# Optimization experiments

Hardware: AMD Instinct MI355X
Metric: run time of the kernel (lower is better)

## Reference

```python
import jax, jax.numpy as jnp
import numpy as np

N, Lq, Lk = 4, 4096, 4096
H, P = 16, 128
D = H * P  # 2048


def setup_inputs() -> dict:
    key = jax.random.key(0)
    ks = jax.random.split(key, 7)
    s = 1.0 / np.sqrt(D).astype(np.float32)
    query = jax.random.normal(ks[0], (N, Lq, D), jnp.float32)
    key_t = jax.random.normal(ks[1], (N, Lk, D), jnp.float32)
    Wq = jax.random.normal(ks[2], (D, D), jnp.float32) * s
    Wk = jax.random.normal(ks[3], (D, D), jnp.float32) * s
    Wv = jax.random.normal(ks[4], (D, D), jnp.float32) * s
    query_padding_mask = jax.random.uniform(ks[5], (N, Lq)) < 0.1
    key_padding_mask = jax.random.uniform(ks[6], (N, Lk)) < 0.1
    return {"query": query, "key": key_t, "Wq": Wq, "Wk": Wk, "Wv": Wv,
            "query_padding_mask": query_padding_mask,
            "key_padding_mask": key_padding_mask}


def reference(query, key, Wq, Wk, Wv, query_padding_mask, key_padding_mask):
    n, lq, _ = query.shape
    lk = key.shape[1]
    # torch.nn.Linear(bias=False): y = x @ W^T; split into heads -> (N,H,L,P)
    q = (query @ Wq.T).reshape(n, lq, H, P).transpose(0, 2, 1, 3)
    k = (key @ Wk.T).reshape(n, lk, H, P).transpose(0, 2, 1, 3)
    v = (key @ Wv.T).reshape(n, lk, H, P).transpose(0, 2, 1, 3)
    # _log_exp_kernel(x) = log(1 + exp(x)) = softplus
    pq = jax.nn.softplus(q)
    pk = jax.nn.softplus(k)
    # zero out padded keys so they contribute nothing to numerator/denominator
    pk = jnp.where(key_padding_mask[:, None, :, None], 0.0, pk)
    # linear attention: O(L*d^2) instead of O(L^2*d)
    kv = jnp.einsum("nhkd,nhke->nhde", pk, v)          # (N,H,P,P)
    num = jnp.einsum("nhqd,nhde->nhqe", pq, kv)        # (N,H,Lq,P)
    den = jnp.einsum("nhqd,nhd->nhq", pq, pk.sum(axis=2))[..., None]
    att = num / den
    out = att.transpose(0, 2, 1, 3).reshape(n, lq, H * P)
    # zero out padded query positions
    out = jnp.where(query_padding_mask[..., None], 0.0, out)
    return out
```

## Files before the change

kernel.cpp:

```cpp
#include <hip/hip_runtime.h>
#include <stdint.h>

typedef __attribute__((ext_vector_type(8))) short    bh8;
typedef __attribute__((ext_vector_type(4))) float    fx4;
typedef __attribute__((ext_vector_type(4))) float    f4v;
typedef unsigned short u16;
typedef __attribute__((ext_vector_type(4))) unsigned short u16x4;

#define DEV static __device__ __forceinline__

DEV u16 f2bf(float f) {
  unsigned u = __float_as_uint(f);
  u += 0x7FFFu + ((u >> 16) & 1u);
  return (u16)(u >> 16);
}
DEV float bf2f(u16 s) { return __uint_as_float(((unsigned)s) << 16); }
DEV float softplus_f(float x) { return fmaxf(x, 0.f) + log1pf(expf(-fabsf(x))); }

DEV void gload_lds16(const u16* g, u16* l) {
  __builtin_amdgcn_global_load_lds(
      (const __attribute__((address_space(1))) unsigned int*)g,
      (__attribute__((address_space(3))) unsigned int*)l, 16, 0, 0);
}
DEV void stage2(const u16* s, u16* d) {
  gload_lds16(s, d);
  gload_lds16(s + 131072, d + 4096);
}

__global__ __launch_bounds__(256) void k_cvt_all(
    const float* __restrict__ q, const float* __restrict__ k,
    const float* __restrict__ wq, const float* __restrict__ wk,
    const float* __restrict__ wv, u16* __restrict__ dst) {
  const int N4 = 19922944;
  int i = blockIdx.x * 256 + threadIdx.x;
  int stride = gridDim.x * 256;
  for (; i < N4; i += stride) {
    const float* src; int off;
    if (i < 8388608)        { src = q;  off = i; }
    else if (i < 16777216)  { src = k;  off = i - 8388608; }
    else if (i < 17825792)  { src = wq; off = i - 16777216; }
    else if (i < 18874368)  { src = wk; off = i - 17825792; }
    else                    { src = wv; off = i - 18874368; }
    f4v v = ((const f4v*)src)[off];
    u16x4 o;
    o.x = f2bf(v.x); o.y = f2bf(v.y); o.z = f2bf(v.z); o.w = f2bf(v.w);
    ((u16x4*)dst)[i] = o;
  }
}


#define MM(a, b, c) __builtin_amdgcn_mfma_f32_16x16x32_bf16(a, b, c, 0, 0, 0)
#define LD(BASE, RR, KS) \
  (*(const bh8*)&lsg[(BASE) + (RR) * 64 + ((((KS) * 32) + ko8) ^ swz)])

#define DECLQ(Q)                                                          \
  fx4 acc##Q##00 = {}, acc##Q##01 = {}, acc##Q##10 = {}, acc##Q##11 = {}, \
      acc##Q##20 = {}, acc##Q##21 = {}, acc##Q##30 = {}, acc##Q##31 = {}

#define DECLFRAGS                                                         \
  bh8 a_00 = {}, a_01 = {}, a_10 = {}, a_11 = {},                         \
      a_20 = {}, a_21 = {}, a_30 = {}, a_31 = {};                         \
  bh8 b0_00 = {}, b0_01 = {}, b0_10 = {}, b0_11 = {};                     \
  bh8 b1_00 = {}, b1_01 = {}, b1_10 = {}, b1_11 = {};

#define LDA4(AB, KS)                                                     \
  a_0##KS = LD(AB, arow0,      KS); a_1##KS = LD(AB, arow0 + 16, KS);    \
  a_2##KS = LD(AB, arow0 + 32, KS); a_3##KS = LD(AB, arow0 + 48, KS);

#define LDB2(BN, BB, KS)                                                 \
  b##BN##_0##KS = LD(BB, brow0,      KS);                                \
  b##BN##_1##KS = LD(BB, brow0 + 16, KS);

#define MFMA8(Q, BN, KS)                                                 \
  acc##Q##00 = MM(a_0##KS, b##BN##_0##KS, acc##Q##00);                   \
  acc##Q##01 = MM(a_0##KS, b##BN##_1##KS, acc##Q##01);                   \
  acc##Q##10 = MM(a_1##KS, b##BN##_0##KS, acc##Q##10);                   \
  acc##Q##11 = MM(a_1##KS, b##BN##_1##KS, acc##Q##11);                   \
  acc##Q##20 = MM(a_2##KS, b##BN##_0##KS, acc##Q##20);                   \
  acc##Q##21 = MM(a_2##KS, b##BN##_1##KS, acc##Q##21);                   \
  acc##Q##30 = MM(a_3##KS, b##BN##_0##KS, acc##Q##30);                   \
  acc##Q##31 = MM(a_3##KS, b##BN##_1##KS, acc##Q##31);

#define KREGION(ABASE, BBASE, DA, DB, SA, SB) {                          \
  stage2(SA,            lsu + (DA));                                     \
  stage2((SA) + 262144, lsu + (DA) + 8192);                              \
  stage2(SB,            lsu + (DB));                                     \
  stage2((SB) + 262144, lsu + (DB) + 8192);                              \
  LDA4(ABASE, 0) LDA4(ABASE, 1)                                          \
  LDB2(0, BBASE, 0) LDB2(0, BBASE, 1)                                    \
  LDB2(1, (BBASE) + 8192, 0) LDB2(1, (BBASE) + 8192, 1)                  \
  __builtin_amdgcn_s_setprio(1);                                         \
  MFMA8(0, 0, 0) MFMA8(0, 0, 1) MFMA8(1, 1, 0) MFMA8(1, 1, 1)            \
  LDA4((ABASE) + 8192, 0) LDA4((ABASE) + 8192, 1)                        \
  MFMA8(2, 0, 0) MFMA8(2, 0, 1) MFMA8(3, 1, 0) MFMA8(3, 1, 1)            \
  __builtin_amdgcn_s_setprio(0);                                         \
  asm volatile("s_waitcnt vmcnt(0)");                                    \
  __builtin_amdgcn_s_barrier();                                          \
}

#define STE(AC, EL, JOFF) {                                                   \
  float v = AC.EL;                                                            \
  if (EPI >= 1) v = softplus_f(v);                                            \
  if (EPI == 2) { if (mask[gi0 + JOFF]) v = 0.f; }                            \
  C[(size_t)(gi0 + JOFF) * 2048 + gj] = f2bf(v);                              \
}
#define ST1(AC, QR, QC, MI, NI) {                                             \
  int gi0 = bm0 + (QR) * 128 + wr * 64 + (MI) * 16 + (lane >> 4) * 4;         \
  int gj  = bn0 + (QC) * 128 + wc * 32 + (NI) * 16 + l15;                     \
  STE(AC, x, 0) STE(AC, y, 1) STE(AC, z, 2) STE(AC, w, 3)                     \
}
#define EPIQ(Q, QR, QC)                                                       \
  ST1(acc##Q##00, QR, QC, 0, 0) ST1(acc##Q##01, QR, QC, 0, 1)                 \
  ST1(acc##Q##10, QR, QC, 1, 0) ST1(acc##Q##11, QR, QC, 1, 1)                 \
  ST1(acc##Q##20, QR, QC, 2, 0) ST1(acc##Q##21, QR, QC, 2, 1)                 \
  ST1(acc##Q##30, QR, QC, 3, 0) ST1(acc##Q##31, QR, QC, 3, 1)

template <int EPI>
__global__ __launch_bounds__(512, 2) void k_gemm256(
    const u16* __restrict__ A, const u16* __restrict__ B, u16* __restrict__ C,
    const int* __restrict__ mask) {
  extern __shared__ u16 lsg[];
  int tid = threadIdx.x, lane = tid & 63, wid = tid >> 6;
  int xcd = blockIdx.x & 7, i = blockIdx.x >> 3;
  int bm0 = (xcd * 8 + (i & 7)) << 8;
  int bn0 = (i >> 3) << 8;
  int wr = wid >> 2, wc = wid & 3;
  int l15 = lane & 15, ko8 = (lane >> 4) * 8;
  int swz = (l15 & 7) << 3;
  int arow0 = wr * 64 + l15, brow0 = wc * 32 + l15;
  int lr = lane >> 3, cg = (lane & 7) ^ lr;
  const u16* srcA = A + (size_t)(bm0 + wid * 8 + lr) * 2048 + cg * 8;
  const u16* srcB = B + (size_t)(bn0 + wid * 8 + lr) * 2048 + cg * 8;
  u16* lsu = lsg + wid * 512;

  DECLQ(0); DECLQ(1); DECLQ(2); DECLQ(3);
  DECLFRAGS

  stage2(srcA,          lsu + 0);
  stage2(srcA + 262144, lsu + 8192);
  stage2(srcB,          lsu + 16384);
  stage2(srcB + 262144, lsu + 24576);
  asm volatile("s_waitcnt vmcnt(0)");
  __builtin_amdgcn_s_barrier();

  for (int it = 0; it < 16; it++) {
    const u16* sA1 = srcA + (2 * it + 1) * 64;
    const u16* sB1 = srcB + (2 * it + 1) * 64;
    int t2 = (2 * it + 2) & 31;
    const u16* sA2 = srcA + t2 * 64;
    const u16* sB2 = srcB + t2 * 64;
    KREGION(0,     16384, 32768, 49152, sA1, sB1)
    KREGION(32768, 49152, 0,     16384, sA2, sB2)
  }

  EPIQ(0, 0, 0)
  EPIQ(1, 0, 1)
  EPIQ(2, 1, 0)
  EPIQ(3, 1, 1)
}

__global__ __launch_bounds__(256, 2) void k_kv2(const u16* __restrict__ pk,
                                                const u16* __restrict__ v,
                                                float* __restrict__ part,
                                                float* __restrict__ spart) {
  int nh = blockIdx.x >> 3, slab = blockIdx.x & 7;
  int n = nh >> 4, h = nh & 15;
  __shared__ u16 lsA[128 * 32];
  __shared__ u16 lsB[128 * 32];
  __shared__ float redS[32][128];
  int tid = threadIdx.x, lane = tid & 63, wid = tid >> 6;
  int wr = wid >> 1, wc = wid & 1;
  int kk = tid >> 3;
  int dg = (tid & 7) * 16;
  size_t rowbase = ((size_t)(n * 4096 + slab * 512) + kk) * 2048 + h * 128 + dg;
  int r = lane & 15, ko = (lane >> 4) * 8;
  fx4 acc[4][4] = {};
  float sA[16];
#pragma unroll
  for (int i = 0; i < 16; i++) sA[i] = 0.f;
  for (int k0 = 0; k0 < 512; k0 += 32) {
    __syncthreads();
    bh8 a0 = *(const bh8*)(pk + rowbase + (size_t)k0 * 2048);
    bh8 a1 = *(const bh8*)(pk + rowbase + (size_t)k0 * 2048 + 8);
    bh8 b0 = *(const bh8*)(v + rowbase + (size_t)k0 * 2048);
    bh8 b1 = *(const bh8*)(v + rowbase + (size_t)k0 * 2048 + 8);
#pragma unroll
    for (int i = 0; i < 8; i++) {
      sA[i] += bf2f((u16)a0[i]);
      sA[8 + i] += bf2f((u16)a1[i]);
    }
#pragma unroll
    for (int i = 0; i < 8; i++) {
      lsA[(dg + i) * 32 + kk] = (u16)a0[i];
      lsA[(dg + 8 + i) * 32 + kk] = (u16)a1[i];
      lsB[(dg + i) * 32 + kk] = (u16)b0[i];
      lsB[(dg + 8 + i) * 32 + kk] = (u16)b1[i];
    }
    __syncthreads();
    bh8 af[4], bfr[4];
#pragma unroll
    for (int mi = 0; mi < 4; mi++)
      af[mi] = *(const bh8*)&lsA[(wr * 64 + mi * 16 + r) * 32 + ko];
#pragma unroll
    for (int ni = 0; ni < 4; ni++)
      bfr[ni] = *(const bh8*)&lsB[(wc * 64 + ni * 16 + r) * 32 + ko];
#pragma unroll
    for (int mi = 0; mi < 4; mi++)
#pragma unroll
      for (int ni = 0; ni < 4; ni++)
        acc[mi][ni] = __builtin_amdgcn_mfma_f32_16x16x32_bf16(af[mi], bfr[ni],
                                                              acc[mi][ni], 0, 0, 0);
  }
#pragma unroll
  for (int mi = 0; mi < 4; mi++)
#pragma unroll
    for (int ni = 0; ni < 4; ni++)
#pragma unroll
      for (int j = 0; j < 4; j++) {
        int d = wr * 64 + mi * 16 + (lane >> 4) * 4 + j;
        int e = wc * 64 + ni * 16 + (lane & 15);
        part[(size_t)blockIdx.x * 16384 + e * 128 + d] = acc[mi][ni][j];
      }
#pragma unroll
  for (int i = 0; i < 16; i++) redS[kk][dg + i] = sA[i];
  __syncthreads();
  if (tid < 128) {
    float s = 0.f;
#pragma unroll
    for (int p = 0; p < 32; p++) s += redS[p][tid];
    spart[blockIdx.x * 128 + tid] = s;
  }
}

__global__ __launch_bounds__(256) void k_red(const float* __restrict__ part,
                                             const float* __restrict__ spart,
                                             u16* __restrict__ kvT,
                                             float* __restrict__ sb) {
  int nh = blockIdx.x, tid = threadIdx.x;
  for (int i = tid; i < 16384; i += 256) {
    float s = 0.f;
#pragma unroll
    for (int sl = 0; sl < 8; sl++) s += part[(size_t)(nh * 8 + sl) * 16384 + i];
    kvT[(size_t)nh * 16384 + i] = f2bf(s);
  }
  if (tid < 128) {
    float s = 0.f;
#pragma unroll
    for (int sl = 0; sl < 8; sl++) s += spart[(nh * 8 + sl) * 128 + tid];
    sb[nh * 128 + tid] = s;
  }
}

__global__ __launch_bounds__(256, 2) void k_att(
    const u16* __restrict__ pq, const u16* __restrict__ kvT,
    const float* __restrict__ s, const int* __restrict__ qmask,
    float* __restrict__ out) {
  int b = blockIdx.x;
  int lt = b & 31, h = (b >> 5) & 15, nb = b >> 9;
  int l0 = lt * 128;
  __shared__ u16 lsQ[128 * 128];
  __shared__ u16 lsKV[128 * 128];
  __shared__ float lsS[128];
  __shared__ float lsDen[128];
  int tid = threadIdx.x, lane = tid & 63, wid = tid >> 6;

  int row = tid >> 1, part = tid & 1;
  const u16* gq = pq + ((size_t)(nb * 4096 + l0 + row)) * 2048 + h * 128 + part * 64;
  const u16* gk = kvT + ((size_t)(nb * 16 + h) * 128 + row) * 128 + part * 64;
  int sw = (row & 7) << 3;
#pragma unroll
  for (int j = 0; j < 8; j++) {
    bh8 vq = *(const bh8*)(gq + j * 8);
    bh8 vk = *(const bh8*)(gk + j * 8);
    int ci = (part * 64 + j * 8) ^ sw;
    *(bh8*)&lsQ[row * 128 + ci] = vq;
    *(bh8*)&lsKV[row * 128 + ci] = vk;
  }
  if (tid < 128) lsS[tid] = s[(nb * 16 + h) * 128 + tid];
  __syncthreads();

  if (tid < 128) {
    int rr = tid, swr = (rr & 7) << 3;
    float dsum = 0.f;
    for (int dd = 0; dd < 128; dd++) {
      int d = (dd + rr) & 127;
      dsum += bf2f(lsQ[rr * 128 + (d ^ swr)]) * lsS[d];
    }
    lsDen[rr] = dsum;
  }
  __syncthreads();

  int wr = wid >> 1, wc = wid & 1;
  int r = lane & 15, ko = (lane >> 4) * 8;
  fx4 acc[4][4] = {};
#pragma unroll
  for (int ks = 0; ks < 4; ks++) {
    bh8 af[4], bfr[4];
#pragma unroll
    for (int mi = 0; mi < 4; mi++) {
      int rw = wr * 64 + mi * 16 + r;
      af[mi] = *(const bh8*)&lsQ[rw * 128 + ((ks * 32 + ko) ^ ((rw & 7) << 3))];
    }
#pragma unroll
    for (int ni = 0; ni < 4; ni++) {
      int rw = wc * 64 + ni * 16 + r;
      bfr[ni] = *(const bh8*)&lsKV[rw * 128 + ((ks * 32 + ko) ^ ((rw & 7) << 3))];
    }
#pragma unroll
    for (int mi = 0; mi < 4; mi++)
#pragma unroll
      for (int ni = 0; ni < 4; ni++)
        acc[mi][ni] = __builtin_amdgcn_mfma_f32_16x16x32_bf16(af[mi], bfr[ni],
                                                              acc[mi][ni], 0, 0, 0);
  }
#pragma unroll
  for (int mi = 0; mi < 4; mi++)
#pragma unroll
    for (int ni = 0; ni < 4; ni++)
#pragma unroll
      for (int j = 0; j < 4; j++) {
        int li = wr * 64 + mi * 16 + (lane >> 4) * 4 + j;
        int e = wc * 64 + ni * 16 + (lane & 15);
        int l = l0 + li;
        float v = qmask[nb * 4096 + l] ? 0.f : acc[mi][ni][j] / lsDen[li];
        out[((size_t)(nb * 4096 + l)) * 2048 + h * 128 + e] = v;
      }
}

extern "C" void kernel_launch(void* const* d_in, const int* in_sizes, int n_in,
                              void* d_out, int out_size, void* d_ws, size_t ws_size,
                              hipStream_t stream) {
  const float* query = (const float*)d_in[0];
  const float* key   = (const float*)d_in[1];
  const float* Wq    = (const float*)d_in[2];
  const float* Wk    = (const float*)d_in[3];
  const float* Wv    = (const float*)d_in[4];
  const int* qmask   = (const int*)d_in[5];
  const int* kmask   = (const int*)d_in[6];
  float* out = (float*)d_out;
  char* ws = (char*)d_ws;

  u16* qb   = (u16*)(ws + 0);
  u16* kb   = (u16*)(ws + 67108864ull);
  u16* Wqb  = (u16*)(ws + 134217728ull);
  u16* Wkb  = (u16*)(ws + 142606336ull);
  u16* Wvb  = (u16*)(ws + 150994944ull);
  u16* pq   = (u16*)(ws + 159383552ull);
  u16* kvT  = (u16*)(ws + 226492416ull);
  float* sb = (float*)(ws + 228589568ull);
  float* kvpart = (float*)(ws + 0);
  float* spart  = (float*)(ws + 33554432ull);
  u16* pk = (u16*)d_out;
  u16* vb = (u16*)d_out + 33554432ull;

  k_cvt_all<<<2048, 256, 0, stream>>>(query, key, Wq, Wk, Wv, qb);

  k_gemm256<1><<<512, 512, 131072, stream>>>(qb, Wqb, pq, nullptr);
  k_gemm256<2><<<512, 512, 131072, stream>>>(kb, Wkb, pk, kmask);
  k_gemm256<0><<<512, 512, 131072, stream>>>(kb, Wvb, vb, nullptr);

  k_kv2<<<512, 256, 0, stream>>>(pk, vb, kvpart, spart);
  k_red<<<64, 256, 0, stream>>>(kvpart, spart, kvT, sb);
  k_att<<<2048, 256, 0, stream>>>(pq, kvT, sb, qmask, out);
}
```

Measured before the change: 732.7 us.

## Add 8-phase ping-pong pipelined GEMM kernel for the query projection

Introduces k_gemm8p, a 256x256-tile bf16 MFMA GEMM that splits each K-step into eight phases. Each phase interleaves LDS fragment reads and the next global-to-LDS stage loads with MFMA bursts, using double-buffered LDS and per-phase barriers. The warp layout gives each wave 128x64 outputs. It replaces the original kernel only for the Q projection, aiming to hide load latency better, at the cost of more barriers and higher register pressure.

```diff
diff --git a/kernel.cpp b/kernel.cpp
--- a/kernel.cpp
+++ b/kernel.cpp
@@ -48,10 +48,139 @@
   }
 }
 
-
 #define MM(a, b, c) __builtin_amdgcn_mfma_f32_16x16x32_bf16(a, b, c, 0, 0, 0)
 #define LD(BASE, RR, KS) \
   (*(const bh8*)&lsg[(BASE) + (RR) * 64 + ((((KS) * 32) + ko8) ^ swz)])
+
+#define STE(AC, EL, JOFF) {                                                   \
+  float v = AC.EL;                                                            \
+  if (EPI >= 1) v = softplus_f(v);                                            \
+  if (EPI == 2) { if (mask[gi0 + JOFF]) v = 0.f; }                            \
+  C[(size_t)(gi0 + JOFF) * 2048 + gj] = f2bf(v);                              \
+}
+
+#define DECLA(G)                                                         \
+  bh8 a##G##_00 = {}, a##G##_01 = {}, a##G##_10 = {}, a##G##_11 = {},    \
+      a##G##_20 = {}, a##G##_21 = {}, a##G##_30 = {}, a##G##_31 = {};
+#define DECLB(J)                                                         \
+  bh8 b##J##_00 = {}, b##J##_01 = {}, b##J##_10 = {}, b##J##_11 = {};
+#define DECLQ8(Q)                                                         \
+  fx4 acc##Q##00 = {}, acc##Q##01 = {}, acc##Q##10 = {}, acc##Q##11 = {}, \
+      acc##Q##20 = {}, acc##Q##21 = {}, acc##Q##30 = {}, acc##Q##31 = {};
+
+#define RDA8(G, BASE, RO)                                                    \
+  a##G##_00 = LD(BASE, arow + (RO),      0);                                 \
+  a##G##_01 = LD(BASE, arow + (RO),      1);                                 \
+  a##G##_10 = LD(BASE, arow + (RO) + 16, 0);                                 \
+  a##G##_11 = LD(BASE, arow + (RO) + 16, 1);                                 \
+  a##G##_20 = LD(BASE, arow + (RO) + 32, 0);                                 \
+  a##G##_21 = LD(BASE, arow + (RO) + 32, 1);                                 \
+  a##G##_30 = LD(BASE, arow + (RO) + 48, 0);                                 \
+  a##G##_31 = LD(BASE, arow + (RO) + 48, 1);
+
+#define RDB4(J, BASE, CO)                                                    \
+  b##J##_00 = LD(BASE, brow + (CO),      0);                                 \
+  b##J##_01 = LD(BASE, brow + (CO),      1);                                 \
+  b##J##_10 = LD(BASE, brow + (CO) + 16, 0);                                 \
+  b##J##_11 = LD(BASE, brow + (CO) + 16, 1);
+
+#define MFQ(G, J, Q)                                                         \
+  acc##Q##00 = MM(a##G##_00, b##J##_00, acc##Q##00);                         \
+  acc##Q##01 = MM(a##G##_00, b##J##_10, acc##Q##01);                         \
+  acc##Q##10 = MM(a##G##_10, b##J##_00, acc##Q##10);                         \
+  acc##Q##11 = MM(a##G##_10, b##J##_10, acc##Q##11);                         \
+  acc##Q##20 = MM(a##G##_20, b##J##_00, acc##Q##20);                         \
+  acc##Q##21 = MM(a##G##_20, b##J##_10, acc##Q##21);                         \
+  acc##Q##30 = MM(a##G##_30, b##J##_00, acc##Q##30);                         \
+  acc##Q##31 = MM(a##G##_30, b##J##_10, acc##Q##31);                         \
+  acc##Q##00 = MM(a##G##_01, b##J##_01, acc##Q##00);                         \
+  acc##Q##01 = MM(a##G##_01, b##J##_11, acc##Q##01);                         \
+  acc##Q##10 = MM(a##G##_11, b##J##_01, acc##Q##10);                         \
+  acc##Q##11 = MM(a##G##_11, b##J##_11, acc##Q##11);                         \
+  acc##Q##20 = MM(a##G##_21, b##J##_01, acc##Q##20);                         \
+  acc##Q##21 = MM(a##G##_21, b##J##_11, acc##Q##21);                         \
+  acc##Q##30 = MM(a##G##_31, b##J##_01, acc##Q##30);                         \
+  acc##Q##31 = MM(a##G##_31, b##J##_11, acc##Q##31);
+
+#define PH8(MFMAS, PRE, ...) {                  \
+  PRE                                           \
+  __VA_ARGS__                                   \
+  __builtin_amdgcn_s_barrier();                 \
+  asm volatile("s_waitcnt lgkmcnt(0)");         \
+  __builtin_amdgcn_s_setprio(1);                \
+  MFMAS                                         \
+  __builtin_amdgcn_s_setprio(0);                \
+}
+#define VM0 asm volatile("s_waitcnt vmcnt(0)");
+
+#define STF(AC, MI, NI, RO, CO) {                                            \
+  int gi0 = bm0 + wr * 128 + (RO) + (MI) * 16 + (lane >> 4) * 4;             \
+  int gj  = bn0 + wc * 64 + (CO) + (NI) * 16 + l15;                          \
+  STE(AC, x, 0) STE(AC, y, 1) STE(AC, z, 2) STE(AC, w, 3)                    \
+}
+#define EPQ8(Q, RO, CO)                                                      \
+  STF(acc##Q##00, 0, 0, RO, CO) STF(acc##Q##01, 0, 1, RO, CO)                \
+  STF(acc##Q##10, 1, 0, RO, CO) STF(acc##Q##11, 1, 1, RO, CO)                \
+  STF(acc##Q##20, 2, 0, RO, CO) STF(acc##Q##21, 2, 1, RO, CO)                \
+  STF(acc##Q##30, 3, 0, RO, CO) STF(acc##Q##31, 3, 1, RO, CO)
+
+template <int EPI>
+__global__ __launch_bounds__(512, 2) void k_gemm8p(
+    const u16* __restrict__ A, const u16* __restrict__ B, u16* __restrict__ C,
+    const int* __restrict__ mask) {
+  extern __shared__ u16 lsg[];
+  int tid = threadIdx.x, lane = tid & 63, wid = tid >> 6;
+  int xcd = blockIdx.x & 7, i = blockIdx.x >> 3;
+  int bm0 = (xcd * 8 + (i & 7)) << 8;
+  int bn0 = (i >> 3) << 8;
+  int wr = wid >> 2, wc = wid & 3;
+  int l15 = lane & 15, ko8 = (lane >> 4) * 8;
+  int swz = (l15 & 7) << 3;
+  int arow = l15;
+  int brow = (wc & 1) * 64 + l15;
+  int abw0 = wr * 8192, abw1 = 32768 + wr * 8192;
+  int bbw0 = 16384 + (wc >> 1) * 8192, bbw1 = 49152 + (wc >> 1) * 8192;
+  int lr = lane >> 3, cg = (lane & 7) ^ lr;
+  const u16* srcA = A + (size_t)(bm0 + wid * 8 + lr) * 2048 + cg * 8;
+  const u16* srcB = B + (size_t)(bn0 + wid * 8 + lr) * 2048 + cg * 8;
+  u16* lsu = lsg + wid * 512;
+
+  DECLQ8(0) DECLQ8(1) DECLQ8(2) DECLQ8(3)
+  DECLA(L) DECLA(H) DECLB(0) DECLB(1)
+
+  stage2(srcA,          lsu + 0);
+  stage2(srcA + 262144, lsu + 8192);
+  stage2(srcB,          lsu + 16384);
+  stage2(srcB + 262144, lsu + 24576);
+  asm volatile("s_waitcnt vmcnt(0)");
+  __builtin_amdgcn_s_barrier();
+
+  for (int it = 0; it < 16; it++) {
+    const u16* sA1 = srcA + (2 * it + 1) * 64;
+    const u16* sB1 = srcB + (2 * it + 1) * 64;
+    int t2 = (2 * it + 2) & 31;
+    const u16* sA2 = srcA + t2 * 64;
+    const u16* sB2 = srcB + t2 * 64;
+    PH8(MFQ(L, 0, 0), ,
+        RDA8(L, abw0, 0) RDB4(0, bbw0, 0)
+        stage2(sA1, lsu + 32768); stage2(sA1 + 262144, lsu + 40960);)
+    PH8(MFQ(L, 1, 1), ,
+        RDB4(1, bbw0, 32)
+        stage2(sB1, lsu + 49152); stage2(sB1 + 262144, lsu + 57344);)
+    PH8(MFQ(H, 0, 2), , RDA8(H, abw0, 64))
+    PH8(MFQ(H, 1, 3), VM0, )
+    PH8(MFQ(L, 0, 0), ,
+        RDA8(L, abw1, 0) RDB4(0, bbw1, 0)
+        stage2(sA2, lsu + 0); stage2(sA2 + 262144, lsu + 8192);)
+    PH8(MFQ(L, 1, 1), ,
+        RDB4(1, bbw1, 32)
+        stage2(sB2, lsu + 16384); stage2(sB2 + 262144, lsu + 24576);)
+    PH8(MFQ(H, 0, 2), , RDA8(H, abw1, 64))
+    PH8(MFQ(H, 1, 3), VM0, )
+  }
+
+  EPQ8(0, 0, 0) EPQ8(1, 0, 32) EPQ8(2, 64, 0) EPQ8(3, 64, 32)
+}
 
 #define DECLQ(Q)                                                          \
   fx4 acc##Q##00 = {}, acc##Q##01 = {}, acc##Q##10 = {}, acc##Q##11 = {}, \
@@ -98,12 +227,6 @@
   __builtin_amdgcn_s_barrier();                                          \
 }
 
-#define STE(AC, EL, JOFF) {                                                   \
-  float v = AC.EL;                                                            \
-  if (EPI >= 1) v = softplus_f(v);                                            \
-  if (EPI == 2) { if (mask[gi0 + JOFF]) v = 0.f; }                            \
-  C[(size_t)(gi0 + JOFF) * 2048 + gj] = f2bf(v);                              \
-}
 #define ST1(AC, QR, QC, MI, NI) {                                             \
   int gi0 = bm0 + (QR) * 128 + wr * 64 + (MI) * 16 + (lane >> 4) * 4;         \
   int gj  = bn0 + (QC) * 128 + wc * 32 + (NI) * 16 + l15;                     \
@@ -355,7 +478,7 @@
 
   k_cvt_all<<<2048, 256, 0, stream>>>(query, key, Wq, Wk, Wv, qb);
 
-  k_gemm256<1><<<512, 512, 131072, stream>>>(qb, Wqb, pq, nullptr);
+  k_gemm8p<1><<<512, 512, 131072, stream>>>(qb, Wqb, pq, nullptr);
   k_gemm256<2><<<512, 512, 131072, stream>>>(kb, Wkb, pk, kmask);
   k_gemm256<0><<<512, 512, 131072, stream>>>(kb, Wvb, vb, nullptr);
 
```

New measurement: 742.9 us. No clear change (+1.4%).
